# Optimization experiments

Hardware: AMD Instinct MI355X
Metric: run time of the kernel (lower is better)

Reference implementation:

```python
import jax, jax.numpy as jnp
from jax import lax
import numpy as np

V, T, K, R, H, EN, L = 10000, 100, 50, 300, 200, 800, 3
B = 128
TRAIN_SIZE = 100000
DELTA = 0.005


def setup_inputs():
    key = jax.random.key(0)
    ks = jax.random.split(key, 16)
    s = 0.02
    return {
        "bows": jax.random.uniform(ks[0], (B, V), jnp.float32) * 10.0 + 1e-3,
        "times": jax.random.randint(ks[1], (B,), 0, T),
        "rnn_inp": jax.random.uniform(ks[2], (T, V), jnp.float32),
        "rho_W": jax.random.normal(ks[3], (V, R), jnp.float32) * s,
        "mu_q_alpha": jax.random.normal(ks[4], (K, T, R), jnp.float32),
        "logsigma_q_alpha": jax.random.normal(ks[5], (K, T, R), jnp.float32) * 0.1 - 2.0,
        "qtheta_W1": jax.random.normal(ks[6], (EN, V + K), jnp.float32) * s,
        "qtheta_b1": jnp.zeros((EN,), jnp.float32),
        "qtheta_W2": jax.random.normal(ks[7], (EN, EN), jnp.float32) * s,
        "qtheta_b2": jnp.zeros((EN,), jnp.float32),
        "mu_theta_W": jax.random.normal(ks[8], (K, EN), jnp.float32) * s,
        "mu_theta_b": jnp.zeros((K,), jnp.float32),
        "ls_theta_W": jax.random.normal(ks[9], (K, EN), jnp.float32) * s,
        "ls_theta_b": jnp.zeros((K,), jnp.float32),
        "eta_map_W": jax.random.normal(ks[10], (H, V), jnp.float32) * s,
        "eta_map_b": jnp.zeros((H,), jnp.float32),
        "lstm_Wih": jax.random.normal(ks[11], (L, 4 * H, H), jnp.float32) * s,
        "lstm_Whh": jax.random.normal(ks[12], (L, 4 * H, H), jnp.float32) * s,
        "lstm_bih": jnp.zeros((L, 4 * H), jnp.float32),
        "lstm_bhh": jnp.zeros((L, 4 * H), jnp.float32),
        "mu_eta_W": jax.random.normal(ks[13], (K, H + K), jnp.float32) * s,
        "mu_eta_b": jnp.zeros((K,), jnp.float32),
        "ls_eta_W": jax.random.normal(ks[14], (K, H + K), jnp.float32) * s,
        "ls_eta_b": jnp.zeros((K,), jnp.float32),
    }


def _kl(q_mu, q_ls, p_mu, p_ls):
    # KL(N(q_mu, exp(q_ls)) || N(p_mu, exp(p_ls))), logsigma == log-variance as in torch code
    return 0.5 * jnp.sum((jnp.exp(q_ls) + (q_mu - p_mu) ** 2) / (jnp.exp(p_ls) + 1e-6) - 1.0 + p_ls - q_ls, axis=-1)


def _lstm(x, Wih, Whh, bih, bhh):
    # x: [T, H]; L stacked LSTM layers (batch of 1 squeezed), torch gate order i,f,g,o
    for l in range(Wih.shape[0]):
        Wi, Wh, bi, bh = Wih[l], Whh[l], bih[l], bhh[l]
        Hd = Wh.shape[1]

        def step(carry, xt, Wi=Wi, Wh=Wh, bi=bi, bh=bh):
            h, c = carry
            g = Wi @ xt + Wh @ h + bi + bh
            i, f, gg, o = jnp.split(g, 4)
            c = jax.nn.sigmoid(f) * c + jax.nn.sigmoid(i) * jnp.tanh(gg)
            h = jax.nn.sigmoid(o) * jnp.tanh(c)
            return (h, c), h

        z = jnp.zeros((Hd,), x.dtype)
        _, x = lax.scan(step, (z, z), x)
    return x


def _forward(bows, rnn_inp, rho_W, mu_q_alpha, logsigma_q_alpha, qtheta_W1, qtheta_b1, qtheta_W2, qtheta_b2, mu_theta_W, mu_theta_b, ls_theta_W, ls_theta_b, eta_map_W, eta_map_b, lstm_Wih, lstm_Whh, lstm_bih, lstm_bhh, mu_eta_W, mu_eta_b, ls_eta_W, ls_eta_b, times):
    log_delta = jnp.log(jnp.float32(DELTA))
    # --- eta: LSTM over word-freq sequence, then sequential mu/logsigma/KL per t ---
    out = _lstm(rnn_inp @ eta_map_W.T + eta_map_b, lstm_Wih, lstm_Whh, lstm_bih, lstm_bhh)  # [T,H]
    p_ls_seq = jnp.concatenate([jnp.zeros((1,), jnp.float32), jnp.full((T - 1,), log_delta, jnp.float32)])

    def eta_step(eta_prev, xs):
        o_t, p_ls = xs
        x = jnp.concatenate([o_t, eta_prev])
        mu = mu_eta_W @ x + mu_eta_b
        ls = ls_eta_W @ x + ls_eta_b
        kl = _kl(mu, ls, eta_prev, jnp.full_like(mu, p_ls))
        return mu, (mu, kl)  # eval-mode reparameterize -> eta_t = mu

    _, (etas, kls) = lax.scan(eta_step, jnp.zeros((K,), jnp.float32), (out, p_ls_seq))
    kl_eta = kls.sum()
    # --- theta encoder ---
    nb = bows / bows.sum(1, keepdims=True)
    eta_td = etas[times]  # [B,K]
    h = jax.nn.relu(jnp.concatenate([nb, eta_td], axis=1) @ qtheta_W1.T + qtheta_b1)
    h = jax.nn.relu(h @ qtheta_W2.T + qtheta_b2)
    mu_t = h @ mu_theta_W.T + mu_theta_b
    ls_t = h @ ls_theta_W.T + ls_theta_b
    theta = jax.nn.softmax(mu_t, axis=-1)  # z = mu (eval-mode reparam)
    coeff = jnp.float32(TRAIN_SIZE / bows.shape[0])
    kl_theta = _kl(mu_t, ls_t, eta_td, jnp.zeros_like(mu_t)).sum() * coeff
    # --- alpha: with eval-mode reparam, alphas == mu, so KL is fully vectorized ---
    muT = jnp.transpose(mu_q_alpha, (1, 0, 2))  # [T,K,R]
    lsT = jnp.transpose(logsigma_q_alpha, (1, 0, 2))
    alphas = muT
    p_mu = jnp.concatenate([jnp.zeros((1, K, R), muT.dtype), alphas[:-1]], axis=0)
    p_ls = jnp.concatenate([jnp.zeros((1, K, R), muT.dtype), jnp.full((T - 1, K, R), log_delta, muT.dtype)], axis=0)
    kl_alpha = _kl(muT, lsT, p_mu, p_ls).sum()
    # --- beta and NLL ---
    logit = alphas.reshape(T * K, R) @ rho_W.T  # [T*K, V]
    beta = jax.nn.softmax(logit, axis=-1).reshape(T, K, V)
    beta_d = beta[times]  # [B,K,V]
    loglik = jnp.log(jnp.einsum('bk,bkv->bv', theta, beta_d) + 1e-12)
    nll = (-(loglik * bows).sum(-1)).sum() * coeff
    loss = nll + kl_eta + kl_theta + kl_alpha
    return loss, nll, kl_eta, kl_theta, kl_alpha


def reference(bows, times, rnn_inp, rho_W, mu_q_alpha, logsigma_q_alpha, qtheta_W1, qtheta_b1, qtheta_W2, qtheta_b2, mu_theta_W, mu_theta_b, ls_theta_W, ls_theta_b, eta_map_W, eta_map_b, lstm_Wih, lstm_Whh, lstm_bih, lstm_bhh, mu_eta_W, mu_eta_b, ls_eta_W, ls_eta_b):
    return _forward(bows, rnn_inp, rho_W, mu_q_alpha, logsigma_q_alpha, qtheta_W1, qtheta_b1, qtheta_W2, qtheta_b2, mu_theta_W, mu_theta_b, ls_theta_W, ls_theta_b, eta_map_W, eta_map_b, lstm_Wih, lstm_Whh, lstm_bih, lstm_bhh, mu_eta_W, mu_eta_b, ls_eta_W, ls_eta_b, times)
```

## Files before the change

kernel.cpp:

```cpp
#include <hip/hip_runtime.h>


typedef unsigned int u32;
typedef unsigned short u16;
typedef _Float16 f16;
typedef f16 f16x2 __attribute__((ext_vector_type(2)));
typedef short bf16x8 __attribute__((ext_vector_type(8)));
typedef float f32x4 __attribute__((ext_vector_type(4)));
typedef u32 u32x4 __attribute__((ext_vector_type(4)));

#define LOG_DELTA (-5.2983174f)
#define COEFF 781.25f

#if defined(__has_builtin)
#if __has_builtin(__builtin_amdgcn_sdot4)
#define HAVE_SDOT4 1
#endif
#endif

__device__ __forceinline__ float bf2f(u16 a) { return __uint_as_float(((u32)a) << 16); }
__device__ __forceinline__ u16 f2bf(float f) {
  u32 u = __float_as_uint(f);
  u32 r = (u + 0x7fffu + ((u >> 16) & 1u)) >> 16;
  return (u16)r;
}
__device__ __forceinline__ int dot4i8(u32 a, u32 b, int c) {
#ifdef HAVE_SDOT4
  return __builtin_amdgcn_sdot4(a, b, c, false);
#else
  int s = c;
  s += ((int)(a << 24) >> 24) * ((int)(b << 24) >> 24);
  s += ((int)(a << 16) >> 24) * ((int)(b << 16) >> 24);
  s += ((int)(a << 8) >> 24) * ((int)(b << 8) >> 24);
  s += ((int)a >> 24) * ((int)b >> 24);
  return s;
#endif
}
__device__ __forceinline__ float sigm(float x) { return 1.f / (1.f + __expf(-x)); }
__device__ __forceinline__ float ftanh(float x) { float t = __expf(2.f * x); return (t - 1.f) / (t + 1.f); }
__device__ __forceinline__ u16 f2h(float x) { return __builtin_bit_cast(u16, (f16)x); }
__device__ __forceinline__ float h2f(u16 x) { return (float)__builtin_bit_cast(f16, x); }
__device__ __forceinline__ void async_load16(const u16* g, u16* l) {
  __builtin_amdgcn_global_load_lds((const __attribute__((address_space(1))) u32*)g,
                                   (__attribute__((address_space(3))) u32*)l, 16, 0, 0);
}


__global__ __launch_bounds__(64) void k_zero(float* __restrict__ accum) {
  if (threadIdx.x < 8) accum[threadIdx.x] = 0.f;
}

__global__ __launch_bounds__(256) void k_nb(const float* __restrict__ bows, float* __restrict__ nb) {
  __shared__ float red[256];
  const int b = blockIdx.x, tid = threadIdx.x;
  float s = 0.f;
  for (int v = tid; v < 10000; v += 256) s += bows[b * 10000 + v];
  red[tid] = s; __syncthreads();
  for (int o = 128; o > 0; o >>= 1) { if (tid < o) red[tid] += red[tid + o]; __syncthreads(); }
  const float inv = 1.f / red[0];
  for (int v = tid; v < 10000; v += 256) nb[b * 10000 + v] = bows[b * 10000 + v] * inv;
}

__global__ __launch_bounds__(256) void k_bsum(const float* __restrict__ a, const float* __restrict__ b,
                                              float* __restrict__ o, int n) {
  int i = blockIdx.x * 256 + threadIdx.x;
  if (i < n) o[i] = a[i] + b[i];
}

__global__ __launch_bounds__(256) void k_fill(float* __restrict__ C, const float* __restrict__ bias,
                                              int N, int total) {
  for (int i = blockIdx.x * 256 + threadIdx.x; i < total; i += gridDim.x * 256)
    C[i] = bias[i % N];
}

__global__ __launch_bounds__(256) void k_relu(float* __restrict__ C, int total) {
  for (int i = blockIdx.x * 256 + threadIdx.x; i < total; i += gridDim.x * 256) {
    float v = C[i];
    C[i] = v > 0.f ? v : 0.f;
  }
}

__global__ __launch_bounds__(128) void k_stack2(const float* __restrict__ a, const float* __restrict__ b,
                                                float* __restrict__ o) {
  const int t = threadIdx.x;
  if (t < 50) o[t] = a[t];
  else if (t < 100) o[t] = b[t - 50];
}

__global__ __launch_bounds__(64) void k_quant_whh(const float* __restrict__ Whh,
                                                  u32* __restrict__ whq, float* __restrict__ rowscale) {
  const int gr = blockIdx.x;
  const int lane = threadIdx.x;
  __shared__ float wrow[200];
  const float* src = Whh + (size_t)gr * 200;
  float m = 0.f;
  for (int c = lane; c < 200; c += 64) { float v = src[c]; wrow[c] = v; m = fmaxf(m, fabsf(v)); }
  for (int o = 32; o > 0; o >>= 1) m = fmaxf(m, __shfl_down(m, o));
  m = __shfl(m, 0);
  const float qs = (m > 0.f) ? 127.f / m : 0.f;
  __syncthreads();
  const int l = gr / 800, rr = gr - l * 800;
  if (lane < 52) {
    u32 d = 0;
    if (lane < 50) {
#pragma unroll
      for (int b = 0; b < 4; ++b) {
        int q = __float2int_rn(wrow[lane * 4 + b] * qs);
        q = max(-127, min(127, q));
        d |= ((u32)(q & 0xff)) << (8 * b);
      }
    }
    whq[l * 41600 + rr * 52 + lane] = d;
  }
  if (lane == 0) rowscale[gr] = (m > 0.f) ? m / 127.f : 0.f;
}

__global__ __launch_bounds__(256) void k_prep_A(const float* __restrict__ muq, u16* __restrict__ Abf) {
  int idx = blockIdx.x * 256 + threadIdx.x;
  if (idx >= 5120 * 320) return;
  int r = idx % 320, m = idx / 320;
  float v = 0.f;
  if (r < 300 && m < 5000) { int t = m / 50, k = m - t * 50; v = muq[k * 30000 + t * 300 + r]; }
  Abf[idx] = f2bf(v);
}
__global__ __launch_bounds__(256) void k_prep_B(const float* __restrict__ rho, u16* __restrict__ Bbf) {
  int idx = blockIdx.x * 256 + threadIdx.x;
  if (idx >= 10112 * 320) return;
  int r = idx % 320, n = idx / 320;
  float v = (r < 300 && n < 10000) ? rho[n * 300 + r] : 0.f;
  Bbf[idx] = f2bf(v);
}


#define ST 64
#define SBK 32

template<int AMODE, int BMODE, int EPI>
__global__ __launch_bounds__(256) void gemm64(
    const float* __restrict__ A, const float* __restrict__ Bm, const float* __restrict__ Bm2,
    const float* __restrict__ bias, float* __restrict__ C,
    int M, int N, int Kd, int lda, int ldb,
    const int* __restrict__ times, const float* __restrict__ etas)
{
  __shared__ __align__(16) float As[SBK][ST + 4];
  __shared__ __align__(16) float Bs[SBK][ST + 4];
  const int tid = threadIdx.x;
  const int tx = tid & 15, ty = tid >> 4;
  const int m_base = blockIdx.x * ST, n_base = blockIdx.y * ST;
  float acc[4][4] = {};
  const int nkt = (Kd + SBK - 1) / SBK;
  const int per = (nkt + gridDim.z - 1) / gridDim.z;
  const int kt0 = blockIdx.z * per;
  const int kt1 = min(nkt, kt0 + per);
  const int lkk = tid & 31;
  const int lrow = tid >> 5;
  for (int kt = kt0; kt < kt1; ++kt) {
    const int kg = kt * SBK + lkk;
#pragma unroll
    for (int i = 0; i < 8; ++i) {
      const int m = m_base + lrow + i * 8;
      float v = 0.f;
      if (m < M && kg < Kd) {
        if (AMODE == 0) v = A[(size_t)m * lda + kg];
        else {
          if (kg < 10000) v = A[(size_t)m * 10000 + kg];
          else v = etas[times[m] * 50 + (kg - 10000)];
        }
      }
      As[lkk][lrow + i * 8] = v;
    }
#pragma unroll
    for (int i = 0; i < 8; ++i) {
      const int n = n_base + lrow + i * 8;
      float v = 0.f;
      if (n < N && kg < Kd) {
        if (BMODE == 0) v = Bm[(size_t)n * ldb + kg];
        else v = (n < 50) ? Bm[(size_t)n * ldb + kg] : Bm2[(size_t)(n - 50) * ldb + kg];
      }
      Bs[lkk][lrow + i * 8] = v;
    }
    __syncthreads();
#pragma unroll
    for (int kk = 0; kk < SBK; ++kk) {
      const float4 a4 = *(const float4*)&As[kk][ty * 4];
      const float4 b4 = *(const float4*)&Bs[kk][tx * 4];
      const float av[4] = {a4.x, a4.y, a4.z, a4.w};
      const float bv[4] = {b4.x, b4.y, b4.z, b4.w};
#pragma unroll
      for (int i = 0; i < 4; ++i)
#pragma unroll
        for (int j = 0; j < 4; ++j) acc[i][j] += av[i] * bv[j];
    }
    __syncthreads();
  }
#pragma unroll
  for (int i = 0; i < 4; ++i) {
    const int m = m_base + ty * 4 + i;
    if (m >= M) continue;
#pragma unroll
    for (int j = 0; j < 4; ++j) {
      const int n = n_base + tx * 4 + j;
      if (n >= N) continue;
      float v = acc[i][j];
      if (EPI == 1) { C[(size_t)m * N + n] = v + bias[n]; }
      else if (EPI == 2) { v += bias[n]; C[(size_t)m * N + n] = v > 0.f ? v : 0.f; }
      else if (EPI == 5) { atomicAdd(&C[(size_t)m * N + n], v); }
      else { C[(size_t)m * N + n] = v; }
    }
  }
}


#define LT 128
#define LBK 32

template<int AMODE>
__global__ __launch_bounds__(256) void gemm128(
    const float* __restrict__ A, const float* __restrict__ Bm,
    float* __restrict__ C,
    int M, int N, int Kd, int lda, int ldb,
    const int* __restrict__ times, const float* __restrict__ etas)
{
  __shared__ __align__(16) float As[LBK][LT + 4];
  __shared__ __align__(16) float Bs[LBK][LT + 4];
  const int tid = threadIdx.x;
  const int tx = tid & 15, ty = tid >> 4;
  const int m_base = blockIdx.x * LT, n_base = blockIdx.y * LT;
  const int nkt = (Kd + LBK - 1) / LBK;
  const int per = (nkt + gridDim.z - 1) / gridDim.z;
  const int kt0 = blockIdx.z * per;
  const int kt1 = min(nkt, kt0 + per);
  if (kt0 >= kt1) return;
  const int lkk = tid & 31;
  const int lrow = tid >> 5;
  float acc[8][8] = {};
  float pa[16], pb[16];
  {
    const int kg = kt0 * LBK + lkk;
#pragma unroll
    for (int i = 0; i < 16; ++i) {
      const int m = m_base + lrow + i * 8;
      float v = 0.f;
      if (m < M && kg < Kd) {
        if (AMODE == 0) v = A[(size_t)m * lda + kg];
        else v = (kg < 10000) ? A[(size_t)m * 10000 + kg] : etas[times[m] * 50 + (kg - 10000)];
      }
      pa[i] = v;
      const int n = n_base + lrow + i * 8;
      float w = 0.f;
      if (n < N && kg < Kd) w = Bm[(size_t)n * ldb + kg];
      pb[i] = w;
    }
  }
  for (int kt = kt0; kt < kt1; ++kt) {
#pragma unroll
    for (int i = 0; i < 16; ++i) {
      As[lkk][lrow + i * 8] = pa[i];
      Bs[lkk][lrow + i * 8] = pb[i];
    }
    __syncthreads();
    if (kt + 1 < kt1) {
      const int kg = (kt + 1) * LBK + lkk;
#pragma unroll
      for (int i = 0; i < 16; ++i) {
        const int m = m_base + lrow + i * 8;
        float v = 0.f;
        if (m < M && kg < Kd) {
          if (AMODE == 0) v = A[(size_t)m * lda + kg];
          else v = (kg < 10000) ? A[(size_t)m * 10000 + kg] : etas[times[m] * 50 + (kg - 10000)];
        }
        pa[i] = v;
        const int n = n_base + lrow + i * 8;
        float w = 0.f;
        if (n < N && kg < Kd) w = Bm[(size_t)n * ldb + kg];
        pb[i] = w;
      }
    }
#pragma unroll
    for (int kk = 0; kk < LBK; ++kk) {
      const float4* ap = (const float4*)&As[kk][ty * 8];
      const float4* bp = (const float4*)&Bs[kk][tx * 8];
      const float4 a0 = ap[0], a1 = ap[1];
      const float4 b0 = bp[0], b1 = bp[1];
      const float av[8] = {a0.x, a0.y, a0.z, a0.w, a1.x, a1.y, a1.z, a1.w};
      const float bv[8] = {b0.x, b0.y, b0.z, b0.w, b1.x, b1.y, b1.z, b1.w};
#pragma unroll
      for (int i = 0; i < 8; ++i)
#pragma unroll
        for (int j = 0; j < 8; ++j) acc[i][j] += av[i] * bv[j];
    }
    __syncthreads();
  }
#pragma unroll
  for (int i = 0; i < 8; ++i) {
    const int m = m_base + ty * 8 + i;
    if (m >= M) continue;
#pragma unroll
    for (int j = 0; j < 8; ++j) {
      const int n = n_base + tx * 8 + j;
      if (n >= N) continue;
      atomicAdd(&C[(size_t)m * N + n], acc[i][j]);
    }
  }
}


__global__ __launch_bounds__(256) void gemm_mfma_bT(
    const u16* __restrict__ A, const u16* __restrict__ B, u16* __restrict__ C,
    int M, int N)
{
  __shared__ u16 As[128 * 32];
  __shared__ u16 Bs[128 * 32];
  const int tid = threadIdx.x;
  const int l = tid & 63, w = tid >> 6;
  const int wm = w & 1, wn = w >> 1;
  const int m0 = blockIdx.x * 128, n0 = blockIdx.y * 128;
  f32x4 acc[4][4] = {};
  const int arow = l >> 2;
  const int acol = (l & 3) * 8;
  for (int kt = 0; kt < 10; ++kt) {
    const int k0 = kt * 32;
#pragma unroll
    for (int c = 0; c < 2; ++c) {
      const int i = w + c * 4;
      async_load16(A + (size_t)(m0 + i * 16 + arow) * 320 + k0 + acol, As + i * 512);
      async_load16(B + (size_t)(n0 + i * 16 + arow) * 320 + k0 + acol, Bs + i * 512);
    }
    __syncthreads();
    bf16x8 af[4], bfr[4];
#pragma unroll
    for (int x = 0; x < 4; ++x) {
      af[x]  = *(const bf16x8*)&As[(wm * 64 + x * 16 + (l & 15)) * 32 + (l >> 4) * 8];
      bfr[x] = *(const bf16x8*)&Bs[(wn * 64 + x * 16 + (l & 15)) * 32 + (l >> 4) * 8];
    }
#pragma unroll
    for (int x = 0; x < 4; ++x)
#pragma unroll
      for (int y = 0; y < 4; ++y)
        acc[x][y] = __builtin_amdgcn_mfma_f32_16x16x32_bf16(af[x], bfr[y], acc[x][y], 0, 0, 0);
    __syncthreads();
  }
  const int col = l & 15, quad = l >> 4;
#pragma unroll
  for (int x = 0; x < 4; ++x) {
    const int gmB = m0 + wm * 64 + x * 16 + quad * 4;
#pragma unroll
    for (int y = 0; y < 4; ++y) {
      const int gn = n0 + wn * 64 + y * 16 + col;
      if (gn >= N) continue;
#pragma unroll
      for (int r = 0; r < 4; ++r) {
        const int gm = gmB + r;
        if (gm < M) C[(size_t)gm * N + gn] = f2bf(acc[x][y][r]);
      }
    }
  }
}


__global__ __launch_bounds__(512, 1) void lstm_scan_reg(
    const u32* __restrict__ whq,
    const float* __restrict__ rowscale,
    const float* __restrict__ xproj,
    float* __restrict__ hseq)
{
  __shared__ u16 pg[800];
  __shared__ __align__(16) u32 hq[52];
  __shared__ float wmax[8];
  __shared__ float hscale_s[1];
  const int tid = threadIdx.x;
  const int act = (tid < 400);
  const int r0 = tid, r1 = tid + 400;
  u32x4 wA4[13], wB4[13];
  float rsA = 0.f, rsB = 0.f;
  float xpA = 0.f, xpB = 0.f;
  if (act) {
    const u32x4* gA = (const u32x4*)(whq + (size_t)r0 * 52);
    const u32x4* gB = (const u32x4*)(whq + (size_t)r1 * 52);
#pragma unroll
    for (int i = 0; i < 13; ++i) { wA4[i] = gA[i]; wB4[i] = gB[i]; }
    rsA = rowscale[r0]; rsB = rowscale[r1];
    xpA = xproj[r0]; xpB = xproj[r1];
  }
  if (tid < 52) hq[tid] = 0;
  if (tid < 8) wmax[tid] = 0.f;
  if (tid == 0) hscale_s[0] = 0.f;
  float c_reg = 0.f;
  __syncthreads();
  for (int t = 0; t < 100; ++t) {
    if (act) {
      float nxA = 0.f, nxB = 0.f;
      if (t < 99) { nxA = xproj[(t + 1) * 800 + r0]; nxB = xproj[(t + 1) * 800 + r1]; }
      const float hdq = hscale_s[0];
      u32x4 hv4[13];
#pragma unroll
      for (int i = 0; i < 13; ++i) hv4[i] = *((const u32x4*)hq + i);
      int aA = 0, aB = 0;
#pragma unroll
      for (int g = 0; g < 50; ++g) {
        const u32 h = hv4[g >> 2][g & 3];
        aA = dot4i8(wA4[g >> 2][g & 3], h, aA);
        aB = dot4i8(wB4[g >> 2][g & 3], h, aB);
      }
      pg[r0] = f2h((float)aA * (rsA * hdq) + xpA);
      pg[r1] = f2h((float)aB * (rsB * hdq) + xpB);
      xpA = nxA; xpB = nxB;
    }
    __syncthreads();
    float hv = 0.f;
    if (tid < 200) {
      float gi = sigm(h2f(pg[tid]));
      float gf = sigm(h2f(pg[200 + tid]));
      float gg = ftanh(h2f(pg[400 + tid]));
      float go = sigm(h2f(pg[600 + tid]));
      c_reg = gf * c_reg + gi * gg;
      hv = go * ftanh(c_reg);
      hseq[t * 200 + tid] = hv;
    }
    float m = fabsf(hv);
    for (int o = 32; o > 0; o >>= 1) m = fmaxf(m, __shfl_down(m, o));
    if ((tid & 63) == 0) wmax[tid >> 6] = m;
    __syncthreads();
    if (tid < 200) {
      const float hm = fmaxf(fmaxf(wmax[0], wmax[1]), fmaxf(wmax[2], wmax[3]));
      const float qs = (hm > 0.f) ? 127.f / hm : 0.f;
      int q = __float2int_rn(hv * qs);
      q = max(-127, min(127, q));
      ((signed char*)hq)[tid] = (signed char)q;
      if (tid == 0) hscale_s[0] = (hm > 0.f) ? hm / 127.f : 0.f;
    }
    __syncthreads();
  }
}


__global__ __launch_bounds__(64, 1) void eta_scan_reg(
    const float* __restrict__ muW, const float* __restrict__ lsW,
    const float* __restrict__ pc0,
    float* __restrict__ etas, float* __restrict__ accum)
{
  __shared__ __align__(16) float ep[52];
  const int j = threadIdx.x;
  const int act = (j < 50);
  float wmu[52], wls[52];
  if (act) {
#pragma unroll
    for (int k = 0; k < 25; ++k) {
      float2 a = *(const float2*)(muW + (size_t)j * 250 + 200 + 2 * k);
      float2 b = *(const float2*)(lsW + (size_t)j * 250 + 200 + 2 * k);
      wmu[2 * k] = a.x; wmu[2 * k + 1] = a.y;
      wls[2 * k] = b.x; wls[2 * k + 1] = b.y;
    }
    wmu[50] = wmu[51] = wls[50] = wls[51] = 0.f;
  } else {
#pragma unroll
    for (int k = 0; k < 52; ++k) { wmu[k] = 0.f; wls[k] = 0.f; }
  }
  if (j < 52) ep[j] = 0.f;
  float klacc = 0.f;
  float mye = 0.f;
  float pmu = act ? pc0[j] : 0.f;
  float pls_ = act ? pc0[50 + j] : 0.f;
  __syncthreads();
  for (int t = 0; t < 100; ++t) {
    float nmu = 0.f, nls = 0.f;
    if (act && t < 99) { nmu = pc0[(t + 1) * 100 + j]; nls = pc0[(t + 1) * 100 + 50 + j]; }
    float ma[4] = {pmu, 0.f, 0.f, 0.f};
    float la[4] = {pls_, 0.f, 0.f, 0.f};
    const float4* e4 = (const float4*)ep;
#pragma unroll
    for (int i = 0; i < 13; ++i) {
      const float4 e = e4[i];
      ma[0] += wmu[4 * i + 0] * e.x; ma[1] += wmu[4 * i + 1] * e.y;
      ma[2] += wmu[4 * i + 2] * e.z; ma[3] += wmu[4 * i + 3] * e.w;
      la[0] += wls[4 * i + 0] * e.x; la[1] += wls[4 * i + 1] * e.y;
      la[2] += wls[4 * i + 2] * e.z; la[3] += wls[4 * i + 3] * e.w;
    }
    const float mu = (ma[0] + ma[1]) + (ma[2] + ma[3]);
    const float ls = (la[0] + la[1]) + (la[2] + la[3]);
    __syncthreads();
    if (act) {
      const float pls = (t == 0) ? 0.f : LOG_DELTA;
      const float pv = __expf(pls) + 1e-6f;
      const float d = mu - mye;
      klacc += 0.5f * ((__expf(ls) + d * d) / pv - 1.f + pls - ls);
      etas[t * 50 + j] = mu;
      mye = mu;
      ep[j] = mu;
    }
    __syncthreads();
    pmu = nmu; pls_ = nls;
  }
  for (int o = 32; o > 0; o >>= 1) klacc += __shfl_down(klacc, o);
  if (j == 0) accum[0] = klacc;
}


__global__ __launch_bounds__(64) void k_theta(const float* __restrict__ mul,
                                              const float* __restrict__ etas, const int* __restrict__ times,
                                              float* __restrict__ theta, float* __restrict__ accum) {
  const int b = blockIdx.x, lane = threadIdx.x;
  float m_ = 0.f, l_ = 0.f, e_ = 0.f, mx = -1e30f;
  if (lane < 50) {
    m_ = mul[b * 100 + lane];
    l_ = mul[b * 100 + 50 + lane];
    e_ = etas[times[b] * 50 + lane];
    mx = m_;
  }
  for (int o = 32; o > 0; o >>= 1) mx = fmaxf(mx, __shfl_down(mx, o));
  mx = __shfl(mx, 0);
  float ex = (lane < 50) ? __expf(m_ - mx) : 0.f;
  float sum = ex;
  for (int o = 32; o > 0; o >>= 1) sum += __shfl_down(sum, o);
  sum = __shfl(sum, 0);
  if (lane < 50) theta[b * 50 + lane] = ex / sum;
  float kl = 0.f;
  if (lane < 50) {
    float d = m_ - e_;
    kl = 0.5f * ((__expf(l_) + d * d) / (1.f + 1e-6f) - 1.f - l_);
  }
  for (int o = 32; o > 0; o >>= 1) kl += __shfl_down(kl, o);
  if (lane == 0) atomicAdd(accum + 1, kl);
}


__global__ __launch_bounds__(256) void k_rowsum(const u16* __restrict__ logit, float* __restrict__ Z) {
  const int r = blockIdx.x, tid = threadIdx.x;
  const u32* row = (const u32*)(logit + (size_t)r * 10000);
  __shared__ float red[256];
  float s = 0.f;
  for (int v = tid; v < 5000; v += 256) {
    u32 p = row[v];
    s += __expf(bf2f((u16)(p & 0xffffu))) + __expf(bf2f((u16)(p >> 16)));
  }
  red[tid] = s; __syncthreads();
  for (int o = 128; o > 0; o >>= 1) { if (tid < o) red[tid] += red[tid + o]; __syncthreads(); }
  if (tid == 0) Z[r] = red[0];
}


__global__ __launch_bounds__(256) void k_nll(const u16* __restrict__ logit, const float* __restrict__ Z,
                                             const float* __restrict__ theta, const float* __restrict__ bows,
                                             const int* __restrict__ times, float* __restrict__ accum) {
  const int b = blockIdx.x, seg = blockIdx.y, tid = threadIdx.x;
  const int t = times[b];
  __shared__ float c2[52];
  __shared__ float red[256];
  if (tid < 50) c2[tid] = theta[b * 50 + tid] / Z[t * 50 + tid];
  __syncthreads();
  float part = 0.f;
  const int v0 = seg * 1250, v1 = v0 + 1250;
  const u16* base = logit + (size_t)t * 500000;
  for (int v = v0 + tid; v < v1; v += 256) {
    float ssv = 1e-12f;
#pragma unroll
    for (int k = 0; k < 50; ++k) ssv += c2[k] * __expf(bf2f(base[k * 10000 + v]));
    part += bows[b * 10000 + v] * __logf(ssv);
  }
  red[tid] = part; __syncthreads();
  for (int o = 128; o > 0; o >>= 1) { if (tid < o) red[tid] += red[tid + o]; __syncthreads(); }
  if (tid == 0) atomicAdd(accum + 3, -red[0]);
}


__global__ __launch_bounds__(256) void k_alpha_kl(const float* __restrict__ muq, const float* __restrict__ lsq,
                                                  float* __restrict__ accum) {
  __shared__ float red[256];
  const int tid = threadIdx.x;
  float s = 0.f;
  for (int i = blockIdx.x * 256 + tid; i < 1500000; i += gridDim.x * 256) {
    int r = i % 300;
    int tk = i / 300;
    int k = tk % 50;
    int t = tk / 50;
    size_t idx = (size_t)k * 30000 + (size_t)t * 300 + r;
    float mu = muq[idx], ls = lsq[idx];
    float pm = 0.f, pls = 0.f;
    if (t > 0) { pm = muq[idx - 300]; pls = LOG_DELTA; }
    float d = mu - pm;
    s += 0.5f * ((__expf(ls) + d * d) / (__expf(pls) + 1e-6f) - 1.f + pls - ls);
  }
  red[tid] = s; __syncthreads();
  for (int o = 128; o > 0; o >>= 1) { if (tid < o) red[tid] += red[tid + o]; __syncthreads(); }
  if (tid == 0) atomicAdd(accum + 2, red[0]);
}


__global__ __launch_bounds__(64) void k_final(const float* __restrict__ accum, float* __restrict__ out) {
  if (threadIdx.x == 0) {
    float nll = accum[3] * COEFF;
    float kl_eta = accum[0];
    float kl_theta = accum[1] * COEFF;
    float kl_alpha = accum[2];
    out[0] = nll + kl_eta + kl_theta + kl_alpha;
    out[1] = nll;
    out[2] = kl_eta;
    out[3] = kl_theta;
    out[4] = kl_alpha;
  }
}


extern "C" void kernel_launch(void* const* d_in, const int* in_sizes, int n_in,
                              void* d_out, int out_size, void* d_ws, size_t ws_size,
                              hipStream_t stream) {
  (void)in_sizes; (void)n_in; (void)out_size; (void)ws_size;
  const float* bows   = (const float*)d_in[0];
  const int*   times  = (const int*)d_in[1];
  const float* rnn_in = (const float*)d_in[2];
  const float* rho_W  = (const float*)d_in[3];
  const float* muq    = (const float*)d_in[4];
  const float* lsq    = (const float*)d_in[5];
  const float* qW1    = (const float*)d_in[6];
  const float* qb1    = (const float*)d_in[7];
  const float* qW2    = (const float*)d_in[8];
  const float* qb2    = (const float*)d_in[9];
  const float* muthW  = (const float*)d_in[10];
  const float* muthb  = (const float*)d_in[11];
  const float* lsthW  = (const float*)d_in[12];
  const float* lsthb  = (const float*)d_in[13];
  const float* emW    = (const float*)d_in[14];
  const float* emb    = (const float*)d_in[15];
  const float* Wih    = (const float*)d_in[16];
  const float* Whh    = (const float*)d_in[17];
  const float* bih    = (const float*)d_in[18];
  const float* bhh    = (const float*)d_in[19];
  const float* mueW   = (const float*)d_in[20];
  const float* mueb   = (const float*)d_in[21];
  const float* lseW   = (const float*)d_in[22];
  const float* lseb   = (const float*)d_in[23];
  float* out = (float*)d_out;
  float* ws = (float*)d_ws;

  float* accum = ws + 0;
  float* nb    = ws + 8;
  float* x0    = ws + 1280008;
  float* xproj = ws + 1300008;
  float* hsA   = ws + 1380008;
  float* hsB   = ws + 1400008;
  u32*   whq   = (u32*)(ws + 1420008);
  float* rowsc = ws + 1544808;
  float* bias2 = ws + 1547208;
  float* pc0   = ws + 1547408;
  float* bias2e= ws + 1558008;
  float* hsC   = ws + 1560008;
  float* bsum  = ws + 1660008;
  float* etas  = ws + 1662408;
  float* h1    = ws + 1667408;
  float* h2    = ws + 1769808;
  float* mul   = ws + 1872208;
  float* theta = ws + 1885008;
  float* Zrow  = ws + 1891408;
  u16*   A_bf  = (u16*)(ws + 1896408);
  u16*   B_bf  = (u16*)(ws + 2715608);
  u16*   logit = (u16*)(ws + 4333528);

  k_zero<<<1, 64, 0, stream>>>(accum);
  k_nb<<<128, 256, 0, stream>>>(bows, nb);
  k_quant_whh<<<2400, 64, 0, stream>>>(Whh, whq, rowsc);
  k_bsum<<<10, 256, 0, stream>>>(bih, bhh, bsum, 2400);
  k_prep_A<<<6400, 256, 0, stream>>>(muq, A_bf);
  k_prep_B<<<12640, 256, 0, stream>>>(rho_W, B_bf);
  k_stack2<<<1, 128, 0, stream>>>(muthb, lsthb, bias2);
  k_stack2<<<1, 128, 0, stream>>>(mueb, lseb, bias2e);
  k_fill<<<40, 256, 0, stream>>>(pc0, bias2e, 100, 10000);

  k_fill<<<79, 256, 0, stream>>>(x0, emb, 200, 20000);
  gemm128<0><<<dim3(1, 2, 104), 256, 0, stream>>>(rnn_in, emW, x0,
                                                  100, 200, 10000, 10000, 10000, nullptr, nullptr);

  const float* lin[3] = {x0, hsA, hsB};
  float* lout[3] = {hsA, hsB, hsC};
  for (int l = 0; l < 3; ++l) {
    gemm64<0, 0, 1><<<dim3(2, 13, 1), 256, 0, stream>>>(lin[l], Wih + l * 160000, nullptr,
                                                        bsum + l * 800, xproj,
                                                        100, 800, 200, 200, 200, nullptr, nullptr);
    lstm_scan_reg<<<1, 512, 0, stream>>>(whq + l * 41600, rowsc + l * 800, xproj, lout[l]);
  }
  gemm64<0, 1, 5><<<dim3(2, 2, 7), 256, 0, stream>>>(hsC, mueW, lseW, nullptr, pc0,
                                                     100, 100, 200, 200, 250, nullptr, nullptr);
  eta_scan_reg<<<1, 64, 0, stream>>>(mueW, lseW, pc0, etas, accum);

  k_fill<<<400, 256, 0, stream>>>(h1, qb1, 800, 102400);
  gemm128<2><<<dim3(1, 7, 45), 256, 0, stream>>>(nb, qW1, h1,
                                                 128, 800, 10050, 10000, 10050, times, etas);
  k_relu<<<400, 256, 0, stream>>>(h1, 102400);
  k_fill<<<400, 256, 0, stream>>>(h2, qb2, 800, 102400);
  gemm64<0, 0, 5><<<dim3(2, 13, 4), 256, 0, stream>>>(h1, qW2, nullptr, nullptr, h2,
                                                      128, 800, 800, 800, 800, nullptr, nullptr);
  k_relu<<<400, 256, 0, stream>>>(h2, 102400);
  k_fill<<<50, 256, 0, stream>>>(mul, bias2, 100, 12800);
  gemm64<0, 1, 5><<<dim3(2, 2, 5), 256, 0, stream>>>(h2, muthW, lsthW, nullptr, mul,
                                                     128, 100, 800, 800, 800, nullptr, nullptr);
  k_theta<<<128, 64, 0, stream>>>(mul, etas, times, theta, accum);

  gemm_mfma_bT<<<dim3(40, 79), 256, 0, stream>>>(A_bf, B_bf, logit, 5000, 10000);
  k_rowsum<<<5000, 256, 0, stream>>>(logit, Zrow);
  k_nll<<<dim3(128, 8), 256, 0, stream>>>(logit, Zrow, theta, bows, times, accum);

  k_alpha_kl<<<512, 256, 0, stream>>>(muq, lsq, accum);
  k_final<<<1, 64, 0, stream>>>(accum, out);
}
```

Measured before the change: 1.337 ms.

## Replace atomic split-K accumulation with partial buffers and fused reduce epilogue

The split-K fp32 GEMMs now write per-slice partial results to separate workspace buffers instead of issuing atomicAdd into a pre-filled output. A new reduction kernel sums the slices, adds the bias and applies ReLU, which replaces the separate fill and relu launches. The embedding GEMM's split count drops from 104 to 64, and the second encoder layer moves from gemm64 to gemm128p. This removes atomic contention and several small launches, but adds partial-buffer memory traffic and reuses the logit workspace region for the partials.

```diff
diff --git a/kernel.cpp b/kernel.cpp
--- a/kernel.cpp
+++ b/kernel.cpp
@@ -73,18 +73,24 @@
     C[i] = bias[i % N];
 }
 
-__global__ __launch_bounds__(256) void k_relu(float* __restrict__ C, int total) {
-  for (int i = blockIdx.x * 256 + threadIdx.x; i < total; i += gridDim.x * 256) {
-    float v = C[i];
-    C[i] = v > 0.f ? v : 0.f;
-  }
-}
-
 __global__ __launch_bounds__(128) void k_stack2(const float* __restrict__ a, const float* __restrict__ b,
                                                 float* __restrict__ o) {
   const int t = threadIdx.x;
   if (t < 50) o[t] = a[t];
   else if (t < 100) o[t] = b[t - 50];
+}
+
+template<int EPI>
+__global__ __launch_bounds__(256) void k_reduceZ(const float* __restrict__ P,
+                                                 const float* __restrict__ bias,
+                                                 float* __restrict__ out,
+                                                 int N, int total, int Z) {
+  for (int i = blockIdx.x * 256 + threadIdx.x; i < total; i += gridDim.x * 256) {
+    float s = bias[i % N];
+    for (int z = 0; z < Z; ++z) s += P[(size_t)z * total + i];
+    if (EPI == 2) s = s > 0.f ? s : 0.f;
+    out[i] = s;
+  }
 }
 
 __global__ __launch_bounds__(64) void k_quant_whh(const float* __restrict__ Whh,
@@ -215,9 +221,9 @@
 #define LBK 32
 
 template<int AMODE>
-__global__ __launch_bounds__(256) void gemm128(
+__global__ __launch_bounds__(256) void gemm128p(
     const float* __restrict__ A, const float* __restrict__ Bm,
-    float* __restrict__ C,
+    float* __restrict__ P,
     int M, int N, int Kd, int lda, int ldb,
     const int* __restrict__ times, const float* __restrict__ etas)
 {
@@ -230,7 +236,6 @@
   const int per = (nkt + gridDim.z - 1) / gridDim.z;
   const int kt0 = blockIdx.z * per;
   const int kt1 = min(nkt, kt0 + per);
-  if (kt0 >= kt1) return;
   const int lkk = tid & 31;
   const int lrow = tid >> 5;
   float acc[8][8] = {};
@@ -291,6 +296,7 @@
     }
     __syncthreads();
   }
+  float* Cz = P + (size_t)blockIdx.z * M * N;
 #pragma unroll
   for (int i = 0; i < 8; ++i) {
     const int m = m_base + ty * 8 + i;
@@ -299,7 +305,7 @@
     for (int j = 0; j < 8; ++j) {
       const int n = n_base + tx * 8 + j;
       if (n >= N) continue;
-      atomicAdd(&C[(size_t)m * N + n], acc[i][j]);
+      Cz[(size_t)m * N + n] = acc[i][j];
     }
   }
 }
@@ -654,6 +660,9 @@
   u16*   A_bf  = (u16*)(ws + 1896408);
   u16*   B_bf  = (u16*)(ws + 2715608);
   u16*   logit = (u16*)(ws + 4333528);
+  float* P1    = ws + 4333528;
+  float* Px0   = ws + 8941528;
+  float* P2    = ws + 10221528;
 
   k_zero<<<1, 64, 0, stream>>>(accum);
   k_nb<<<128, 256, 0, stream>>>(bows, nb);
@@ -665,9 +674,9 @@
   k_stack2<<<1, 128, 0, stream>>>(mueb, lseb, bias2e);
   k_fill<<<40, 256, 0, stream>>>(pc0, bias2e, 100, 10000);
 
-  k_fill<<<79, 256, 0, stream>>>(x0, emb, 200, 20000);
-  gemm128<0><<<dim3(1, 2, 104), 256, 0, stream>>>(rnn_in, emW, x0,
+  gemm128p<0><<<dim3(1, 2, 64), 256, 0, stream>>>(rnn_in, emW, Px0,
                                                   100, 200, 10000, 10000, 10000, nullptr, nullptr);
+  k_reduceZ<1><<<79, 256, 0, stream>>>(Px0, emb, x0, 200, 20000, 64);
 
   const float* lin[3] = {x0, hsA, hsB};
   float* lout[3] = {hsA, hsB, hsC};
@@ -681,14 +690,12 @@
                                                      100, 100, 200, 200, 250, nullptr, nullptr);
   eta_scan_reg<<<1, 64, 0, stream>>>(mueW, lseW, pc0, etas, accum);
 
-  k_fill<<<400, 256, 0, stream>>>(h1, qb1, 800, 102400);
-  gemm128<2><<<dim3(1, 7, 45), 256, 0, stream>>>(nb, qW1, h1,
-                                                 128, 800, 10050, 10000, 10050, times, etas);
-  k_relu<<<400, 256, 0, stream>>>(h1, 102400);
-  k_fill<<<400, 256, 0, stream>>>(h2, qb2, 800, 102400);
-  gemm64<0, 0, 5><<<dim3(2, 13, 4), 256, 0, stream>>>(h1, qW2, nullptr, nullptr, h2,
-                                                      128, 800, 800, 800, 800, nullptr, nullptr);
-  k_relu<<<400, 256, 0, stream>>>(h2, 102400);
+  gemm128p<2><<<dim3(1, 7, 45), 256, 0, stream>>>(nb, qW1, P1,
+                                                  128, 800, 10050, 10000, 10050, times, etas);
+  k_reduceZ<2><<<400, 256, 0, stream>>>(P1, qb1, h1, 800, 102400, 45);
+  gemm128p<0><<<dim3(1, 7, 5), 256, 0, stream>>>(h1, qW2, P2,
+                                                 128, 800, 800, 800, 800, nullptr, nullptr);
+  k_reduceZ<2><<<400, 256, 0, stream>>>(P2, qb2, h2, 800, 102400, 5);
   k_fill<<<50, 256, 0, stream>>>(mul, bias2, 100, 12800);
   gemm64<0, 1, 5><<<dim3(2, 2, 5), 256, 0, stream>>>(h2, muthW, lsthW, nullptr, mul,
                                                      128, 100, 800, 800, 800, nullptr, nullptr);
```

Result: faster. 1.109 ms (-17.0%).
